# Kernel optimization log

Measured on AMD Instinct MI355X. Metric: run time of the kernel, lower is better.

## Reference

```python
import jax, jax.numpy as jnp
import numpy as np

B, H, W = 512, 30, 30
NUM_COLORS, IN_DIM, HID, OUT_DIM, NUM_LAYERS = 10, 12, 128, 64, 4
LN_EPS = 1e-5


def _grid_edge_index(h, w):
    # 4-connectivity, both directions, plus self-loops (PyG GCNConv default add_self_loops=True)
    idx = np.arange(h * w).reshape(h, w)
    src = np.concatenate([idx[:, :-1].ravel(), idx[:, 1:].ravel(),
                          idx[:-1, :].ravel(), idx[1:, :].ravel(), idx.ravel()])
    dst = np.concatenate([idx[:, 1:].ravel(), idx[:, :-1].ravel(),
                          idx[1:, :].ravel(), idx[:-1, :].ravel(), idx.ravel()])
    return np.stack([src, dst]).astype(np.int32)


def setup_inputs() -> dict:
    key = jax.random.key(0)
    ks = jax.random.split(key, 10)
    p = lambda k, shape: (jax.random.normal(k, shape, dtype=jnp.float32) * 0.02)
    grids = jax.random.randint(ks[0], (B, H, W), 0, NUM_COLORS, dtype=jnp.int32)
    return {
        "grids": grids,
        "edge_index": jnp.asarray(_grid_edge_index(H, W)),
        "Win": p(ks[1], (IN_DIM, HID)),
        "bin_": jnp.zeros((HID,), jnp.float32),
        "Wg": p(ks[2], (NUM_LAYERS, HID, HID)),
        "bg": jnp.zeros((NUM_LAYERS, HID), jnp.float32),
        "gamma": jnp.ones((NUM_LAYERS, HID), jnp.float32),
        "beta": jnp.zeros((NUM_LAYERS, HID), jnp.float32),
        "Wout": p(ks[3], (HID, OUT_DIM)),
        "bout": jnp.zeros((OUT_DIM,), jnp.float32),
    }


def _layer_norm(x, g, b):
    m = jnp.mean(x, axis=-1, keepdims=True)
    v = jnp.var(x, axis=-1, keepdims=True)
    return (x - m) * jax.lax.rsqrt(v + LN_EPS) * g + b


def reference(grids, edge_index, Win, bin_, Wg, bg, gamma, beta, Wout, bout):
    Bb, Hh, Ww = grids.shape
    N = Hh * Ww
    src, dst = edge_index[0], edge_index[1]

    # symmetric GCN normalization: D^{-1/2} (A+I) D^{-1/2}
    deg = jax.ops.segment_sum(jnp.ones_like(dst, jnp.float32), dst, num_segments=N)
    dinv = jax.lax.rsqrt(jnp.maximum(deg, 1.0))
    coef = (dinv[src] * dinv[dst])[:, None]  # [E,1]

    # node features: one-hot color + normalized (row, col) positions
    rows = jnp.repeat(jnp.arange(Hh, dtype=jnp.float32) / max(Hh - 1, 1), Ww)
    cols = jnp.tile(jnp.arange(Ww, dtype=jnp.float32) / max(Ww - 1, 1), Hh)
    pos = jnp.stack([rows, cols], axis=-1)  # [N,2]

    def encode(grid_flat):  # grid_flat: [N] int
        feat = jnp.concatenate([jax.nn.one_hot(grid_flat, NUM_COLORS, dtype=jnp.float32), pos], axis=-1)
        x = jax.nn.relu(feat @ Win + bin_)  # [N,HID]
        for i in range(NUM_LAYERS):
            h = x @ Wg[i]
            agg = jax.ops.segment_sum(h[src] * coef, dst, num_segments=N) + bg[i]
            x = jax.nn.relu(_layer_norm(agg, gamma[i], beta[i])) + x
        return x @ Wout + bout  # [N,OUT_DIM]

    return jax.vmap(encode)(grids.reshape(Bb, N))
```

## Files before the change

kernel.cpp:

```cpp
#include <hip/hip_runtime.h>

#define HID 128
#define ODIM 64

typedef _Float16 half8 __attribute__((ext_vector_type(8)));
typedef float f32x4 __attribute__((ext_vector_type(4)));

typedef const __attribute__((address_space(1))) void* as1cvp;
typedef __attribute__((address_space(3))) void* as3vp;

__device__ __forceinline__ void gload16(const void* g, void* l) {
  __builtin_amdgcn_global_load_lds((as1cvp)g, (as3vp)l, 16, 0, 0);
}

__global__ __launch_bounds__(256) void k_prep(
    const float* __restrict__ Wg, const float* __restrict__ Wout,
    _Float16* __restrict__ WspHi, _Float16* __restrict__ WspLo,
    _Float16* __restrict__ WhHi, _Float16* __restrict__ WhLo) {
  int i = blockIdx.x * 256 + threadIdx.x;
  if (i < 65536) {
    int j = i & 7, n = (i >> 3) & 127, g = (i >> 10) & 3, kc = (i >> 12) & 3, l = i >> 14;
    int k = kc * 32 + g * 8 + j;
    float v = Wg[(size_t)(l * 128 + k) * 128 + n];
    WspHi[i] = (_Float16)v;
  } else if (i < 131072) {
    int m = i - 65536;
    int j = m & 7, n = (m >> 3) & 127, g = (m >> 10) & 3, kc = (m >> 12) & 3, l = m >> 14;
    int k = kc * 32 + g * 8 + j;
    float v = Wg[(size_t)(l * 128 + k) * 128 + n];
    _Float16 h = (_Float16)v;
    WspLo[m] = (_Float16)(v - (float)h);
  } else if (i < 139264) {
    int m = i - 131072;
    int j = m & 7, n = (m >> 3) & 63, g = (m >> 9) & 3, kc = m >> 11;
    int k = kc * 32 + g * 8 + j;
    float v = Wout[k * 64 + n];
    WhHi[m] = (_Float16)v;
  } else if (i < 147456) {
    int m = i - 139264;
    int j = m & 7, n = (m >> 3) & 63, g = (m >> 9) & 3, kc = m >> 11;
    int k = kc * 32 + g * 8 + j;
    float v = Wout[k * 64 + n];
    _Float16 h = (_Float16)v;
    WhLo[m] = (_Float16)(v - (float)h);
  }
}

__global__ __launch_bounds__(256) void k_encode(
    const int* __restrict__ grids, const float* __restrict__ Win,
    const float* __restrict__ binp, float* __restrict__ X, int b0, int nodes) {
  int t = blockIdx.x * 256 + threadIdx.x;
  if (t >= nodes * 32) return;
  int node = t >> 5;
  int i = t & 31;
  int n = node % 900;
  int b = node / 900;
  int r = n / 30, c = n - r * 30;
  int color = grids[(b0 + b) * 900 + n];
  float fr = (float)r / 29.0f, fc = (float)c / 29.0f;
  f32x4 wc = ((const f32x4*)(Win + color * HID))[i];
  f32x4 wr = ((const f32x4*)(Win + 10 * HID))[i];
  f32x4 wl = ((const f32x4*)(Win + 11 * HID))[i];
  f32x4 bb = ((const f32x4*)binp)[i];
  f32x4 v = wc + fr * wr + fc * wl + bb;
#pragma unroll
  for (int j = 0; j < 4; ++j) v[j] = fmaxf(v[j], 0.0f);
  ((f32x4*)(X + (size_t)node * HID))[i] = v;
}

__global__ __launch_bounds__(512, 4) void k_hidden(
    const float* __restrict__ Xin, float* __restrict__ Xout,
    const _Float16* __restrict__ Whi, const _Float16* __restrict__ Wlo,
    const float* __restrict__ bgp, const float* __restrict__ gamp,
    const float* __restrict__ betp, int nodesTotal) {
  __shared__ __attribute__((aligned(16))) float Xt[2][192 * 32];
  __shared__ __attribute__((aligned(16))) _Float16 WTh[2][4 * 128 * 8];
  __shared__ __attribute__((aligned(16))) _Float16 WTl[2][4 * 128 * 8];

  const int t = threadIdx.x;
  const int lane = t & 63;
  const int wave = t >> 6;
  const int q = lane >> 4, l16 = lane & 15;

  int nwg = gridDim.x, bid = blockIdx.x;
  int qd = nwg >> 3, rm = nwg & 7;
  int xcd = bid & 7, idx = bid >> 3;
  int wg = (xcd < rm ? xcd * (qd + 1) : rm * (qd + 1) + (xcd - rm) * qd) + idx;
  const int blockRow0 = wg * 128;
  const int waveRow0 = blockRow0 + wave * 16;

  int off[5];
  float wts[5];
  {
    int nd = waveRow0 + l16;
    if (nd > nodesTotal - 1) nd = nodesTotal - 1;
    int n = nd % 900;
    int r = n / 30, c = n - r * 30;
    int loc = nd - blockRow0 + 30;
    int nb[5] = {loc, loc - 30, loc + 30, loc - 1, loc + 1};
    float dc = rsqrtf((float)(1 + (r > 0) + (r < 29) + (c > 0) + (c < 29)));
    wts[0] = dc * dc;
    wts[1] = (r > 0) ? dc * rsqrtf((float)(2 + (r > 1) + (c > 0) + (c < 29))) : 0.f;
    wts[2] = (r < 29) ? dc * rsqrtf((float)(2 + (r < 28) + (c > 0) + (c < 29))) : 0.f;
    wts[3] = (c > 0) ? dc * rsqrtf((float)(2 + (r > 0) + (r < 29) + (c > 1))) : 0.f;
    wts[4] = (c < 29) ? dc * rsqrtf((float)(2 + (r > 0) + (r < 29) + (c < 28))) : 0.f;
#pragma unroll
    for (int e = 0; e < 5; ++e)
      off[e] = nb[e] * 32 + (((2 * q) ^ (nb[e] & 7)) << 2);
  }

  auto stage = [&](int kc, int buf) {
#pragma unroll
    for (int s = 0; s < 3; ++s) {
      int f = t + s * 512;
      int row = f >> 3, v = f & 7;
      int gr = blockRow0 - 30 + row;
      gr = gr < 0 ? 0 : (gr > nodesTotal - 1 ? nodesTotal - 1 : gr);
      gload16(Xin + (size_t)gr * HID + kc * 32 + ((v ^ (row & 7)) << 2),
              &Xt[buf][(s * 512 + wave * 64) * 4]);
    }
    gload16(Whi + kc * 4096 + t * 8, &WTh[buf][wave * 64 * 8]);
    gload16(Wlo + kc * 4096 + t * 8, &WTl[buf][wave * 64 * 8]);
  };

  f32x4 acc[8];
#pragma unroll
  for (int nt = 0; nt < 8; ++nt) acc[nt] = (f32x4){0.f, 0.f, 0.f, 0.f};

  stage(0, 0);
  __syncthreads();

  for (int kc = 0; kc < 4; ++kc) {
    const int cur = kc & 1;
    if (kc < 3) stage(kc + 1, cur ^ 1);

    half8 Ahi, Alo;
    {
      const float* Xb = Xt[cur];
      f32x4 s0 = {0.f, 0.f, 0.f, 0.f}, s1 = {0.f, 0.f, 0.f, 0.f};
#pragma unroll
      for (int e = 0; e < 5; ++e) {
        s0 += wts[e] * (*(const f32x4*)(Xb + off[e]));
        s1 += wts[e] * (*(const f32x4*)(Xb + (off[e] ^ 4)));
      }
#pragma unroll
      for (int j = 0; j < 4; ++j) {
        _Float16 h0 = (_Float16)s0[j];
        Ahi[j] = h0;
        Alo[j] = (_Float16)(s0[j] - (float)h0);
        _Float16 h1 = (_Float16)s1[j];
        Ahi[4 + j] = h1;
        Alo[4 + j] = (_Float16)(s1[j] - (float)h1);
      }
    }
#pragma unroll
    for (int nt = 0; nt < 8; ++nt) {
      int n = nt * 16 + l16;
      half8 bhi = *(const half8*)(&WTh[cur][(q * 128 + n) * 8]);
      half8 blo = *(const half8*)(&WTl[cur][(q * 128 + n) * 8]);
      acc[nt] = __builtin_amdgcn_mfma_f32_16x16x32_f16(Alo, bhi, acc[nt], 0, 0, 0);
      acc[nt] = __builtin_amdgcn_mfma_f32_16x16x32_f16(Ahi, blo, acc[nt], 0, 0, 0);
      acc[nt] = __builtin_amdgcn_mfma_f32_16x16x32_f16(Ahi, bhi, acc[nt], 0, 0, 0);
    }
    if (kc < 3) __syncthreads();
  }

  float bgv[8], gv[8], btv[8];
#pragma unroll
  for (int nt = 0; nt < 8; ++nt) {
    int cl = nt * 16 + l16;
    bgv[nt] = bgp[cl];
    gv[nt] = gamp[cl];
    btv[nt] = betp[cl];
  }
#pragma unroll
  for (int reg = 0; reg < 4; ++reg) {
    float rs = 0.f;
#pragma unroll
    for (int nt = 0; nt < 8; ++nt) {
      acc[nt][reg] += bgv[nt];
      rs += acc[nt][reg];
    }
    rs += __shfl_xor(rs, 1, 64);
    rs += __shfl_xor(rs, 2, 64);
    rs += __shfl_xor(rs, 4, 64);
    rs += __shfl_xor(rs, 8, 64);
    float mean = rs * (1.f / 128.f);
    float ss = 0.f;
#pragma unroll
    for (int nt = 0; nt < 8; ++nt) {
      float d = acc[nt][reg] - mean;
      ss += d * d;
    }
    ss += __shfl_xor(ss, 1, 64);
    ss += __shfl_xor(ss, 2, 64);
    ss += __shfl_xor(ss, 4, 64);
    ss += __shfl_xor(ss, 8, 64);
    float rsd = rsqrtf(ss * (1.f / 128.f) + 1e-5f);
    int row = waveRow0 + q * 4 + reg;
    if (row < nodesTotal) {
      const float* xr = Xin + (size_t)row * HID;
      float* xo = Xout + (size_t)row * HID;
#pragma unroll
      for (int nt = 0; nt < 8; ++nt) {
        int col = nt * 16 + l16;
        float y = fmaxf((acc[nt][reg] - mean) * rsd * gv[nt] + btv[nt], 0.f);
        xo[col] = y + xr[col];
      }
    }
  }
}

__global__ __launch_bounds__(512, 4) void k_head(
    const float* __restrict__ Xin, float* __restrict__ Out,
    const _Float16* __restrict__ Whi, const _Float16* __restrict__ Wlo,
    const float* __restrict__ bp, int nodesTotal) {
  __shared__ __attribute__((aligned(16))) float Xt[2][256 * 32];
  __shared__ __attribute__((aligned(16))) _Float16 WTh[2][4 * 64 * 8];
  __shared__ __attribute__((aligned(16))) _Float16 WTl[2][4 * 64 * 8];

  const int t = threadIdx.x;
  const int lane = t & 63;
  const int wave = t >> 6;
  const int q = lane >> 4, l16 = lane & 15;
  const int blockRow0 = blockIdx.x * 256;
  const int waveRow0 = blockRow0 + wave * 32;

  int off[2];
#pragma unroll
  for (int mt = 0; mt < 2; ++mt) {
    int nd = waveRow0 + mt * 16 + l16;
    if (nd > nodesTotal - 1) nd = nodesTotal - 1;
    int rn = nd - blockRow0;
    off[mt] = rn * 32 + (((2 * q) ^ (rn & 7)) << 2);
  }

  auto stage = [&](int kc, int buf) {
#pragma unroll
    for (int s = 0; s < 4; ++s) {
      int f = t + s * 512;
      int row = f >> 3, v = f & 7;
      int gr = blockRow0 + row;
      if (gr > nodesTotal - 1) gr = nodesTotal - 1;
      gload16(Xin + (size_t)gr * HID + kc * 32 + ((v ^ (row & 7)) << 2),
              &Xt[buf][(s * 512 + wave * 64) * 4]);
    }
    if (t < 256)
      gload16(Whi + kc * 2048 + t * 8, &WTh[buf][wave * 64 * 8]);
    else
      gload16(Wlo + kc * 2048 + (t - 256) * 8, &WTl[buf][(wave - 4) * 64 * 8]);
  };

  f32x4 acc[2][4];
#pragma unroll
  for (int mt = 0; mt < 2; ++mt)
#pragma unroll
    for (int nt = 0; nt < 4; ++nt) acc[mt][nt] = (f32x4){0.f, 0.f, 0.f, 0.f};

  stage(0, 0);
  __syncthreads();

  for (int kc = 0; kc < 4; ++kc) {
    const int cur = kc & 1;
    if (kc < 3) stage(kc + 1, cur ^ 1);

    half8 Ahi[2], Alo[2];
    const float* Xb = Xt[cur];
#pragma unroll
    for (int mt = 0; mt < 2; ++mt) {
      f32x4 s0 = *(const f32x4*)(Xb + off[mt]);
      f32x4 s1 = *(const f32x4*)(Xb + (off[mt] ^ 4));
#pragma unroll
      for (int j = 0; j < 4; ++j) {
        _Float16 h0 = (_Float16)s0[j];
        Ahi[mt][j] = h0;
        Alo[mt][j] = (_Float16)(s0[j] - (float)h0);
        _Float16 h1 = (_Float16)s1[j];
        Ahi[mt][4 + j] = h1;
        Alo[mt][4 + j] = (_Float16)(s1[j] - (float)h1);
      }
    }
#pragma unroll
    for (int nt = 0; nt < 4; ++nt) {
      int n = nt * 16 + l16;
      half8 bhi = *(const half8*)(&WTh[cur][(q * 64 + n) * 8]);
      half8 blo = *(const half8*)(&WTl[cur][(q * 64 + n) * 8]);
#pragma unroll
      for (int mt = 0; mt < 2; ++mt) {
        acc[mt][nt] = __builtin_amdgcn_mfma_f32_16x16x32_f16(Alo[mt], bhi, acc[mt][nt], 0, 0, 0);
        acc[mt][nt] = __builtin_amdgcn_mfma_f32_16x16x32_f16(Ahi[mt], blo, acc[mt][nt], 0, 0, 0);
        acc[mt][nt] = __builtin_amdgcn_mfma_f32_16x16x32_f16(Ahi[mt], bhi, acc[mt][nt], 0, 0, 0);
      }
    }
    if (kc < 3) __syncthreads();
  }

  float bv[4];
#pragma unroll
  for (int nt = 0; nt < 4; ++nt) bv[nt] = bp[nt * 16 + l16];
#pragma unroll
  for (int mt = 0; mt < 2; ++mt) {
#pragma unroll
    for (int reg = 0; reg < 4; ++reg) {
      int row = waveRow0 + mt * 16 + q * 4 + reg;
      if (row < nodesTotal) {
        float* op = Out + (size_t)row * ODIM;
#pragma unroll
        for (int nt = 0; nt < 4; ++nt)
          op[nt * 16 + l16] = acc[mt][nt][reg] + bv[nt];
      }
    }
  }
}

extern "C" void kernel_launch(void* const* d_in, const int* in_sizes, int n_in,
                              void* d_out, int out_size, void* d_ws, size_t ws_size,
                              hipStream_t stream) {
  const int* grids = (const int*)d_in[0];
  const float* Win  = (const float*)d_in[2];
  const float* bin  = (const float*)d_in[3];
  const float* Wg   = (const float*)d_in[4];
  const float* bg   = (const float*)d_in[5];
  const float* gam  = (const float*)d_in[6];
  const float* bet  = (const float*)d_in[7];
  const float* Wout = (const float*)d_in[8];
  const float* bout = (const float*)d_in[9];
  float* Out = (float*)d_out;

  _Float16* WspHi = (_Float16*)d_ws;
  _Float16* WspLo = WspHi + 65536;
  _Float16* WhHi  = WspHi + 131072;
  _Float16* WhLo  = WspHi + 139264;
  const size_t wBytes = 294912;

  const int Btot = 512;
  const size_t perBatchBytes = (size_t)900 * HID * 4 * 2;
  size_t xws = ws_size > wBytes ? ws_size - wBytes : 0;
  int chunkB = (int)(xws / perBatchBytes);
  if (chunkB > Btot) chunkB = Btot;
  if (chunkB < 1) chunkB = 1;
  int nch = (Btot + chunkB - 1) / chunkB;

  float* Xa = (float*)((char*)d_ws + wBytes);
  float* Xb = Xa + (size_t)chunkB * 900 * HID;

  k_prep<<<dim3(576), dim3(256), 0, stream>>>(Wg, Wout, WspHi, WspLo, WhHi, WhLo);

  for (int ci = 0; ci < nch; ++ci) {
    int b0 = ci * chunkB;
    int cb = Btot - b0;
    if (cb > chunkB) cb = chunkB;
    int nodes = cb * 900;
    int gbh = (nodes + 127) / 128;
    int gbo = (nodes + 255) / 256;

    k_encode<<<dim3((nodes * 32 + 255) / 256), dim3(256), 0, stream>>>(
        grids, Win, bin, Xa, b0, nodes);
    float* src = Xa;
    float* dst = Xb;
    for (int l = 0; l < 4; ++l) {
      k_hidden<<<dim3(gbh), dim3(512), 0, stream>>>(
          src, dst, WspHi + l * 16384, WspLo + l * 16384,
          bg + l * HID, gam + l * HID, bet + l * HID, nodes);
      float* tmp = src; src = dst; dst = tmp;
    }
    k_head<<<dim3(gbo), dim3(512), 0, stream>>>(
        src, Out + (size_t)b0 * 900 * ODIM, WhHi, WhLo, bout, nodes);
  }
}
```

Before: 853.8 us.

## Fuse last GCN layer with output head projection in one kernel

Replaces the separate head kernel with a fused kernel that runs the fourth GCN layer (stencil aggregation, MFMA, bias, layernorm, residual) and then, from split-fp16 values kept in shared memory, runs the output projection. This drops one kernel launch and the round trip of the final 128-wide hidden state through global memory. It also remaps block indices across XCDs so adjacent row tiles share a die's cache. In exchange it uses more shared memory and registers per block, and the head weights are read straight from global memory.

```diff
diff --git a/kernel.cpp b/kernel.cpp
--- a/kernel.cpp
+++ b/kernel.cpp
@@ -211,51 +211,67 @@
   }
 }
 
-__global__ __launch_bounds__(512, 4) void k_head(
-    const float* __restrict__ Xin, float* __restrict__ Out,
+__global__ __launch_bounds__(512, 4) void k_hidden3(
+    const float* __restrict__ Xin, float* __restrict__ Outp,
     const _Float16* __restrict__ Whi, const _Float16* __restrict__ Wlo,
-    const float* __restrict__ bp, int nodesTotal) {
-  __shared__ __attribute__((aligned(16))) float Xt[2][256 * 32];
-  __shared__ __attribute__((aligned(16))) _Float16 WTh[2][4 * 64 * 8];
-  __shared__ __attribute__((aligned(16))) _Float16 WTl[2][4 * 64 * 8];
+    const float* __restrict__ bgp, const float* __restrict__ gamp,
+    const float* __restrict__ betp, const _Float16* __restrict__ WhHig,
+    const _Float16* __restrict__ WhLog, const float* __restrict__ boutp,
+    int nodesTotal) {
+  __shared__ __attribute__((aligned(16))) char smem[81920];
+  float* XtB = (float*)smem;
+  _Float16* WThB = (_Float16*)(smem + 49152);
+  _Float16* WTlB = (_Float16*)(smem + 65536);
 
   const int t = threadIdx.x;
   const int lane = t & 63;
   const int wave = t >> 6;
   const int q = lane >> 4, l16 = lane & 15;
-  const int blockRow0 = blockIdx.x * 256;
-  const int waveRow0 = blockRow0 + wave * 32;
-
-  int off[2];
-#pragma unroll
-  for (int mt = 0; mt < 2; ++mt) {
-    int nd = waveRow0 + mt * 16 + l16;
+
+  int nwg = gridDim.x, bid = blockIdx.x;
+  int qd = nwg >> 3, rm = nwg & 7;
+  int xcd = bid & 7, idx = bid >> 3;
+  int wg = (xcd < rm ? xcd * (qd + 1) : rm * (qd + 1) + (xcd - rm) * qd) + idx;
+  const int blockRow0 = wg * 128;
+  const int waveRow0 = blockRow0 + wave * 16;
+
+  int off[5];
+  float wts[5];
+  {
+    int nd = waveRow0 + l16;
     if (nd > nodesTotal - 1) nd = nodesTotal - 1;
-    int rn = nd - blockRow0;
-    off[mt] = rn * 32 + (((2 * q) ^ (rn & 7)) << 2);
+    int n = nd % 900;
+    int r = n / 30, c = n - r * 30;
+    int loc = nd - blockRow0 + 30;
+    int nb[5] = {loc, loc - 30, loc + 30, loc - 1, loc + 1};
+    float dc = rsqrtf((float)(1 + (r > 0) + (r < 29) + (c > 0) + (c < 29)));
+    wts[0] = dc * dc;
+    wts[1] = (r > 0) ? dc * rsqrtf((float)(2 + (r > 1) + (c > 0) + (c < 29))) : 0.f;
+    wts[2] = (r < 29) ? dc * rsqrtf((float)(2 + (r < 28) + (c > 0) + (c < 29))) : 0.f;
+    wts[3] = (c > 0) ? dc * rsqrtf((float)(2 + (r > 0) + (r < 29) + (c > 1))) : 0.f;
+    wts[4] = (c < 29) ? dc * rsqrtf((float)(2 + (r > 0) + (r < 29) + (c < 28))) : 0.f;
+#pragma unroll
+    for (int e = 0; e < 5; ++e)
+      off[e] = nb[e] * 32 + (((2 * q) ^ (nb[e] & 7)) << 2);
   }
 
   auto stage = [&](int kc, int buf) {
 #pragma unroll
-    for (int s = 0; s < 4; ++s) {
+    for (int s = 0; s < 3; ++s) {
       int f = t + s * 512;
       int row = f >> 3, v = f & 7;
-      int gr = blockRow0 + row;
-      if (gr > nodesTotal - 1) gr = nodesTotal - 1;
+      int gr = blockRow0 - 30 + row;
+      gr = gr < 0 ? 0 : (gr > nodesTotal - 1 ? nodesTotal - 1 : gr);
       gload16(Xin + (size_t)gr * HID + kc * 32 + ((v ^ (row & 7)) << 2),
-              &Xt[buf][(s * 512 + wave * 64) * 4]);
-    }
-    if (t < 256)
-      gload16(Whi + kc * 2048 + t * 8, &WTh[buf][wave * 64 * 8]);
-    else
-      gload16(Wlo + kc * 2048 + (t - 256) * 8, &WTl[buf][(wave - 4) * 64 * 8]);
+              XtB + buf * 6144 + (s * 512 + wave * 64) * 4);
+    }
+    gload16(Whi + kc * 4096 + t * 8, WThB + buf * 4096 + wave * 512);
+    gload16(Wlo + kc * 4096 + t * 8, WTlB + buf * 4096 + wave * 512);
   };
 
-  f32x4 acc[2][4];
-#pragma unroll
-  for (int mt = 0; mt < 2; ++mt)
-#pragma unroll
-    for (int nt = 0; nt < 4; ++nt) acc[mt][nt] = (f32x4){0.f, 0.f, 0.f, 0.f};
+  f32x4 acc[8];
+#pragma unroll
+  for (int nt = 0; nt < 8; ++nt) acc[nt] = (f32x4){0.f, 0.f, 0.f, 0.f};
 
   stage(0, 0);
   __syncthreads();
@@ -264,51 +280,120 @@
     const int cur = kc & 1;
     if (kc < 3) stage(kc + 1, cur ^ 1);
 
-    half8 Ahi[2], Alo[2];
-    const float* Xb = Xt[cur];
-#pragma unroll
-    for (int mt = 0; mt < 2; ++mt) {
-      f32x4 s0 = *(const f32x4*)(Xb + off[mt]);
-      f32x4 s1 = *(const f32x4*)(Xb + (off[mt] ^ 4));
+    half8 Ahi, Alo;
+    {
+      const float* Xb = XtB + cur * 6144;
+      f32x4 s0 = {0.f, 0.f, 0.f, 0.f}, s1 = {0.f, 0.f, 0.f, 0.f};
+#pragma unroll
+      for (int e = 0; e < 5; ++e) {
+        s0 += wts[e] * (*(const f32x4*)(Xb + off[e]));
+        s1 += wts[e] * (*(const f32x4*)(Xb + (off[e] ^ 4)));
+      }
 #pragma unroll
       for (int j = 0; j < 4; ++j) {
         _Float16 h0 = (_Float16)s0[j];
-        Ahi[mt][j] = h0;
-        Alo[mt][j] = (_Float16)(s0[j] - (float)h0);
+        Ahi[j] = h0;
+        Alo[j] = (_Float16)(s0[j] - (float)h0);
         _Float16 h1 = (_Float16)s1[j];
-        Ahi[mt][4 + j] = h1;
-        Alo[mt][4 + j] = (_Float16)(s1[j] - (float)h1);
-      }
-    }
+        Ahi[4 + j] = h1;
+        Alo[4 + j] = (_Float16)(s1[j] - (float)h1);
+      }
+    }
+#pragma unroll
+    for (int nt = 0; nt < 8; ++nt) {
+      int n = nt * 16 + l16;
+      half8 bhi = *(const half8*)(WThB + cur * 4096 + (q * 128 + n) * 8);
+      half8 blo = *(const half8*)(WTlB + cur * 4096 + (q * 128 + n) * 8);
+      acc[nt] = __builtin_amdgcn_mfma_f32_16x16x32_f16(Alo, bhi, acc[nt], 0, 0, 0);
+      acc[nt] = __builtin_amdgcn_mfma_f32_16x16x32_f16(Ahi, blo, acc[nt], 0, 0, 0);
+      acc[nt] = __builtin_amdgcn_mfma_f32_16x16x32_f16(Ahi, bhi, acc[nt], 0, 0, 0);
+    }
+    __syncthreads();
+  }
+
+  _Float16* Xhi = (_Float16*)smem;
+  _Float16* Xlo = (_Float16*)(smem + 32768);
+  float bgv[8], gv[8], btv[8];
+#pragma unroll
+  for (int nt = 0; nt < 8; ++nt) {
+    int cl = nt * 16 + l16;
+    bgv[nt] = bgp[cl];
+    gv[nt] = gamp[cl];
+    btv[nt] = betp[cl];
+  }
+#pragma unroll
+  for (int reg = 0; reg < 4; ++reg) {
+    float rs = 0.f;
+#pragma unroll
+    for (int nt = 0; nt < 8; ++nt) {
+      acc[nt][reg] += bgv[nt];
+      rs += acc[nt][reg];
+    }
+    rs += __shfl_xor(rs, 1, 64);
+    rs += __shfl_xor(rs, 2, 64);
+    rs += __shfl_xor(rs, 4, 64);
+    rs += __shfl_xor(rs, 8, 64);
+    float mean = rs * (1.f / 128.f);
+    float ss = 0.f;
+#pragma unroll
+    for (int nt = 0; nt < 8; ++nt) {
+      float d = acc[nt][reg] - mean;
+      ss += d * d;
+    }
+    ss += __shfl_xor(ss, 1, 64);
+    ss += __shfl_xor(ss, 2, 64);
+    ss += __shfl_xor(ss, 4, 64);
+    ss += __shfl_xor(ss, 8, 64);
+    float rsd = rsqrtf(ss * (1.f / 128.f) + 1e-5f);
+    int row = waveRow0 + q * 4 + reg;
+    int lr = wave * 16 + q * 4 + reg;
+    if (row < nodesTotal) {
+      const float* xr = Xin + (size_t)row * HID;
+#pragma unroll
+      for (int nt = 0; nt < 8; ++nt) {
+        int col = nt * 16 + l16;
+        float y = fmaxf((acc[nt][reg] - mean) * rsd * gv[nt] + btv[nt], 0.f);
+        float fx = y + xr[col];
+        int sg = (col >> 3) ^ (lr & 7);
+        int pa = lr * 128 + sg * 8 + (col & 7);
+        _Float16 h = (_Float16)fx;
+        Xhi[pa] = h;
+        Xlo[pa] = (_Float16)(fx - (float)h);
+      }
+    }
+  }
+  __syncthreads();
+
+  f32x4 hacc[4];
+#pragma unroll
+  for (int nt = 0; nt < 4; ++nt) hacc[nt] = (f32x4){0.f, 0.f, 0.f, 0.f};
+  const int alr = wave * 16 + l16;
+#pragma unroll
+  for (int kc = 0; kc < 4; ++kc) {
+    int ag = (kc * 4 + q) ^ (alr & 7);
+    half8 ahi = *(const half8*)(Xhi + alr * 128 + ag * 8);
+    half8 alo = *(const half8*)(Xlo + alr * 128 + ag * 8);
 #pragma unroll
     for (int nt = 0; nt < 4; ++nt) {
       int n = nt * 16 + l16;
-      half8 bhi = *(const half8*)(&WTh[cur][(q * 64 + n) * 8]);
-      half8 blo = *(const half8*)(&WTl[cur][(q * 64 + n) * 8]);
-#pragma unroll
-      for (int mt = 0; mt < 2; ++mt) {
-        acc[mt][nt] = __builtin_amdgcn_mfma_f32_16x16x32_f16(Alo[mt], bhi, acc[mt][nt], 0, 0, 0);
-        acc[mt][nt] = __builtin_amdgcn_mfma_f32_16x16x32_f16(Ahi[mt], blo, acc[mt][nt], 0, 0, 0);
-        acc[mt][nt] = __builtin_amdgcn_mfma_f32_16x16x32_f16(Ahi[mt], bhi, acc[mt][nt], 0, 0, 0);
-      }
-    }
-    if (kc < 3) __syncthreads();
-  }
-
+      half8 bhi = *(const half8*)(WhHig + kc * 2048 + q * 512 + n * 8);
+      half8 blo = *(const half8*)(WhLog + kc * 2048 + q * 512 + n * 8);
+      hacc[nt] = __builtin_amdgcn_mfma_f32_16x16x32_f16(alo, bhi, hacc[nt], 0, 0, 0);
+      hacc[nt] = __builtin_amdgcn_mfma_f32_16x16x32_f16(ahi, blo, hacc[nt], 0, 0, 0);
+      hacc[nt] = __builtin_amdgcn_mfma_f32_16x16x32_f16(ahi, bhi, hacc[nt], 0, 0, 0);
+    }
+  }
   float bv[4];
 #pragma unroll
-  for (int nt = 0; nt < 4; ++nt) bv[nt] = bp[nt * 16 + l16];
-#pragma unroll
-  for (int mt = 0; mt < 2; ++mt) {
-#pragma unroll
-    for (int reg = 0; reg < 4; ++reg) {
-      int row = waveRow0 + mt * 16 + q * 4 + reg;
-      if (row < nodesTotal) {
-        float* op = Out + (size_t)row * ODIM;
-#pragma unroll
-        for (int nt = 0; nt < 4; ++nt)
-          op[nt * 16 + l16] = acc[mt][nt][reg] + bv[nt];
-      }
+  for (int nt = 0; nt < 4; ++nt) bv[nt] = boutp[nt * 16 + l16];
+#pragma unroll
+  for (int reg = 0; reg < 4; ++reg) {
+    int row = waveRow0 + q * 4 + reg;
+    if (row < nodesTotal) {
+      float* op = Outp + (size_t)row * ODIM;
+#pragma unroll
+      for (int nt = 0; nt < 4; ++nt)
+        op[nt * 16 + l16] = hacc[nt][reg] + bv[nt];
     }
   }
 }
@@ -352,19 +437,19 @@
     if (cb > chunkB) cb = chunkB;
     int nodes = cb * 900;
     int gbh = (nodes + 127) / 128;
-    int gbo = (nodes + 255) / 256;
 
     k_encode<<<dim3((nodes * 32 + 255) / 256), dim3(256), 0, stream>>>(
         grids, Win, bin, Xa, b0, nodes);
     float* src = Xa;
     float* dst = Xb;
-    for (int l = 0; l < 4; ++l) {
+    for (int l = 0; l < 3; ++l) {
       k_hidden<<<dim3(gbh), dim3(512), 0, stream>>>(
           src, dst, WspHi + l * 16384, WspLo + l * 16384,
           bg + l * HID, gam + l * HID, bet + l * HID, nodes);
       float* tmp = src; src = dst; dst = tmp;
     }
-    k_head<<<dim3(gbo), dim3(512), 0, stream>>>(
-        src, Out + (size_t)b0 * 900 * ODIM, WhHi, WhLo, bout, nodes);
-  }
-}
+    k_hidden3<<<dim3(gbh), dim3(512), 0, stream>>>(
+        src, Out + (size_t)b0 * 900 * ODIM, WspHi + 3 * 16384, WspLo + 3 * 16384,
+        bg + 3 * HID, gam + 3 * HID, bet + 3 * HID, WhHi, WhLo, bout, nodes);
+  }
+}
```

Result: faster. 825.5 us (-3.3%).
